# Kernel tuning notes

Measured on AMD Instinct MI355X. Metric: run time of the kernel, lower is better.

Reference implementation:

```python
import jax, jax.numpy as jnp
import numpy as np

A, M, KA, KB = 100000, 200000, 6, 5  # atoms, messages, agraph width, bgraph width
D, DB, H = 256, 256, 256             # atom embed, bond embed, hidden
DEPTH, ATOMS, BONDS = 4, 120, 4


def setup_inputs() -> dict:
    key = jax.random.key(0)
    ks = jax.random.split(key, 14)
    f32 = jnp.float32

    def lin(k, o, i):
        s = 1.0 / np.sqrt(i)
        return jax.random.uniform(k, (o, i), f32, -s, s)

    return dict(
        E_a=jax.random.normal(ks[0], (ATOMS, D), f32) * 0.1,
        E_b=jax.random.normal(ks[1], (BONDS, DB), f32) * 0.1,
        Wz_w=lin(ks[2], H, D + DB + H), Wz_b=jnp.zeros((H,), f32),
        Wr_w=lin(ks[3], H, D + DB),
        Ur_w=lin(ks[4], H, H), Ur_b=jnp.zeros((H,), f32),
        Wh_w=lin(ks[5], H, D + DB + H), Wh_b=jnp.zeros((H,), f32),
        O1_w=lin(ks[6], H, D + H), O1_b=jnp.zeros((H,), f32),
        O2_w=lin(ks[7], H, H), O2_b=jnp.zeros((H,), f32),
        fnode=jax.random.randint(ks[8], (A,), 0, ATOMS),
        fmess_src=jax.random.randint(ks[9], (M,), 0, A),
        fmess_bond=jax.random.randint(ks[10], (M,), 0, BONDS),
        agraph=jax.random.randint(ks[11], (A, KA), 0, M),
        bgraph=jax.random.randint(ks[12], (M, KB), 0, M),
        depth=DEPTH,
    )


def reference(E_a, E_b, Wz_w, Wz_b, Wr_w, Ur_w, Ur_b, Wh_w, Wh_b,
              O1_w, O1_b, O2_w, O2_b,
              fnode, fmess_src, fmess_bond, agraph, bgraph, depth):
    # embed_graph: atom features + message input features
    hnode = E_a[fnode]                                           # [A, D]
    x = jnp.concatenate([hnode[fmess_src], E_b[fmess_bond]], -1)  # [M, D+DB]

    m = x.shape[0]
    h = jnp.zeros((m, Wz_b.shape[0]), x.dtype)                   # [M, H]
    mask = jnp.ones((m, 1), x.dtype).at[0].set(0.0)              # msg 0 = padding
    wr_x = x @ Wr_w.T                                            # loop-invariant

    # GRU message passing (JTNN-style), depthG iterations
    for _ in range(depth):
        h_nei = h[bgraph]                                        # [M, KB, H] gather
        sum_h = h_nei.sum(axis=1)
        z = jax.nn.sigmoid(jnp.concatenate([x, sum_h], -1) @ Wz_w.T + Wz_b)
        r = jax.nn.sigmoid(wr_x[:, None, :] + h_nei @ Ur_w.T + Ur_b)
        sum_gated = (r * h_nei).sum(axis=1)
        pre_h = jnp.tanh(jnp.concatenate([x, sum_gated], -1) @ Wh_w.T + Wh_b)
        h = ((1.0 - z) * sum_h + z * pre_h) * mask

    # mpn tail: gather-sum neighbor messages per atom, concat, outputAtom MLP
    mess_nei = h[agraph].sum(axis=1)                             # [A, H]
    nv = jnp.concatenate([hnode, mess_nei], axis=-1)             # [A, D+H]
    out = jax.nn.relu(nv @ O1_w.T + O1_b) @ O2_w.T + O2_b        # [A, H]
    return out
```

## Files before the change

### kernel.cpp

```cpp
#include <hip/hip_runtime.h>

#define MM 200000
#define AA 100000
#define KA 6
#define KB 5
#define NATOM 120
#define NBOND 4
#define NC (NATOM*NBOND)
#define HH 256
#define HU_B 768

typedef unsigned char  u8;
typedef unsigned short ushort_t;
typedef __attribute__((ext_vector_type(8))) short bf16x8;
typedef __attribute__((ext_vector_type(8))) unsigned short u16x8;
typedef __attribute__((ext_vector_type(4))) float f32x4;
typedef __attribute__((ext_vector_type(2))) float f32x2;
typedef __attribute__((ext_vector_type(4))) unsigned int u32x4;
typedef __attribute__((ext_vector_type(2))) unsigned int u32x2;

#define SBAR() __builtin_amdgcn_sched_barrier(0)

#define OFF_Ea   0
#define OFF_Eb   30720
#define OFF_Wz   31744
#define OFF_Wzb  228352
#define OFF_Wr   228608
#define OFF_Ur   359680
#define OFF_Urb  425216
#define OFF_Wh   425472
#define OFF_Whb  622080
#define OFF_O1   622336
#define OFF_O1b  753408
#define OFF_O2   753664
#define OFF_O2b  819200
#define W_TOTAL  819456

__device__ u8       g_hu0[(size_t)MM*HU_B];
__device__ u8       g_hu1[(size_t)MM*HU_B];
__device__ u8       g_tab[481*HU_B];
__device__ ushort_t g_trb[NC*HH];
__device__ float    g_tz[NC*HH];
__device__ float    g_th[NC*HH];
__device__ float    g_to1[NATOM*HH];
__device__ int      g_cidx[MM];
__device__ ushort_t c_w[W_TOTAL];
__device__ int      g_isf32;

__device__ inline float bf2f(ushort_t u){ return __uint_as_float(((unsigned)u)<<16); }
__device__ inline ushort_t f2bf(float f){
  unsigned u = __float_as_uint(f);
  unsigned r = (u + 0x7FFFu + ((u>>16)&1u)) >> 16;
  return (ushort_t)r;
}
__device__ inline float sigm(float x){
  return __builtin_amdgcn_rcpf(1.0f + __expf(-x));
}
__device__ inline float tanh_f(float x){
  float ax = fabsf(x);
  float e = __expf(-2.0f*ax);
  float t = (1.0f - e) * __builtin_amdgcn_rcpf(1.0f + e);
  return copysignf(t, x);
}
__device__ inline int sidx(int row, int col){ return row*256 + (col ^ ((row&7)<<3)); }

__device__ inline bf16x8 ldsA(const ushort_t* tile, int m0, int lane, int k0){
  int row = m0 + (lane & 15);
  int col = k0 + 8*(lane>>4);
  return *(const bf16x8*)(tile + sidx(row, col));
}
__device__ inline bf16x8 ldgB(const ushort_t* W, int ldw, int koff, int n0, int lane, int k0){
  int n = n0 + (lane & 15);
  int k = koff + k0 + 8*(lane>>4);
  return *(const bf16x8*)(W + n*ldw + k);
}
__device__ inline f32x4 mfma16(bf16x8 a, bf16x8 b, f32x4 c){
  return __builtin_amdgcn_mfma_f32_16x16x32_bf16(a, b, c, 0, 0, 0);
}
__device__ inline void st16(u8* p, const ushort_t* lds_src){
  *(u32x4*)p = *(const u32x4*)lds_src;
}
__device__ inline u32x2 enc_fp8x8(const ushort_t* s){
  u32x2 o;
  int w0 = __builtin_amdgcn_cvt_pk_fp8_f32(bf2f(s[0]), bf2f(s[1]), 0, 0);
  w0     = __builtin_amdgcn_cvt_pk_fp8_f32(bf2f(s[2]), bf2f(s[3]), w0, 1);
  int w1 = __builtin_amdgcn_cvt_pk_fp8_f32(bf2f(s[4]), bf2f(s[5]), 0, 0);
  w1     = __builtin_amdgcn_cvt_pk_fp8_f32(bf2f(s[6]), bf2f(s[7]), w1, 1);
  o.x = (unsigned)w0; o.y = (unsigned)w1;
  return o;
}

__global__ __launch_bounds__(256) void k_detect(const ushort_t* Ea_raw){
  __shared__ int sbad;
  if (threadIdx.x == 0) sbad = 0;
  __syncthreads();
  float v = bf2f(Ea_raw[2*threadIdx.x]);
  float av = fabsf(v);
  int bad = (av > 1e4f) || (av != 0.0f && av < 1e-30f);
  atomicAdd(&sbad, bad);
  __syncthreads();
  if (threadIdx.x == 0) g_isf32 = (sbad > 64) ? 1 : 0;
}

__global__ __launch_bounds__(256) void k_convert(
    const void* Ea, const void* Eb, const void* Wz, const void* Wzb,
    const void* Wr, const void* Ur, const void* Urb, const void* Wh,
    const void* Whb, const void* O1, const void* O1b, const void* O2,
    const void* O2b)
{
  int idx = blockIdx.x*256 + threadIdx.x;
  if (idx >= W_TOTAL) return;
  const void* src; int j;
  if      (idx < OFF_Eb)  { src = Ea;  j = idx - OFF_Ea; }
  else if (idx < OFF_Wz)  { src = Eb;  j = idx - OFF_Eb; }
  else if (idx < OFF_Wzb) { src = Wz;  j = idx - OFF_Wz; }
  else if (idx < OFF_Wr)  { src = Wzb; j = idx - OFF_Wzb; }
  else if (idx < OFF_Ur)  { src = Wr;  j = idx - OFF_Wr; }
  else if (idx < OFF_Urb) { src = Ur;  j = idx - OFF_Ur; }
  else if (idx < OFF_Wh)  { src = Urb; j = idx - OFF_Urb; }
  else if (idx < OFF_Whb) { src = Wh;  j = idx - OFF_Wh; }
  else if (idx < OFF_O1)  { src = Whb; j = idx - OFF_Whb; }
  else if (idx < OFF_O1b) { src = O1;  j = idx - OFF_O1; }
  else if (idx < OFF_O2)  { src = O1b; j = idx - OFF_O1b; }
  else if (idx < OFF_O2b) { src = O2;  j = idx - OFF_O2; }
  else                    { src = O2b; j = idx - OFF_O2b; }
  ushort_t v;
  if (g_isf32) v = f2bf(((const float*)src)[j]);
  else         v = ((const ushort_t*)src)[j];
  c_w[idx] = v;
}

__global__ __launch_bounds__(256) void k_tables()
{
  const ushort_t* Ea  = c_w + OFF_Ea;
  const ushort_t* Eb  = c_w + OFF_Eb;
  int b = blockIdx.x, o = threadIdx.x;
  if (b < 3*NC) {
    int t = b / NC, c = b % NC, a = c >> 2, bd = c & 3;
    const ushort_t* W; const ushort_t* bias; int ldw;
    if (t == 0)      { W = c_w + OFF_Wr; bias = c_w + OFF_Urb; ldw = 512; }
    else if (t == 1) { W = c_w + OFF_Wz; bias = c_w + OFF_Wzb; ldw = 768; }
    else             { W = c_w + OFF_Wh; bias = c_w + OFF_Whb; ldw = 768; }
    float acc = bf2f(bias[o]);
    const ushort_t* wrow = W + o*ldw;
    for (int d = 0; d < 256; d++) acc += bf2f(Ea[a*256+d]) * bf2f(wrow[d]);
    for (int d = 0; d < 256; d++) acc += bf2f(Eb[bd*256+d]) * bf2f(wrow[256+d]);
    if (t == 0)      g_trb[c*256 + o] = f2bf(acc);
    else if (t == 1) g_tz[c*256 + o] = acc;
    else             g_th[c*256 + o] = acc;
  } else {
    int a = b - 3*NC;
    float acc = bf2f(c_w[OFF_O1b + o]);
    const ushort_t* wrow = c_w + OFF_O1 + o*512;
    for (int d = 0; d < 256; d++) acc += bf2f(Ea[a*256+d]) * bf2f(wrow[d]);
    g_to1[a*256 + o] = acc;
  }
}

__global__ __launch_bounds__(256) void k_cidx(const int* fnode, const int* fsrc, const int* fbond){
  int m = blockIdx.x*256 + threadIdx.x;
  if (m >= MM) return;
  g_cidx[m] = fnode[fsrc[m]]*4 + fbond[m];
}

__global__ __launch_bounds__(256) void k_tab0(){
  __shared__ ushort_t sh[256];
  int b = blockIdx.x, o = threadIdx.x;
  u8* row = g_tab + (size_t)b*HU_B;
  if (b == 480){
    ((ushort_t*)row)[o] = 0;
    row[512 + o] = 0;
    return;
  }
  float h = sigm(g_tz[b*256+o]) * tanh_f(g_th[b*256+o]);
  ushort_t hb = f2bf(h);
  ((ushort_t*)row)[o] = hb;
  sh[o] = hb;
  __syncthreads();
  const ushort_t* ur = c_w + OFF_Ur + o*256;
  float acc = 0.f;
  for (int d = 0; d < 256; d++) acc += bf2f(sh[d]) * bf2f(ur[d]);
  int pk = __builtin_amdgcn_cvt_pk_fp8_f32(acc, acc, 0, 0);
  row[512 + o] = (u8)(pk & 0xFF);
}

__global__ __launch_bounds__(256,4) void k_fused(const int* __restrict__ bgraph, int rd, int tbl, int last){
  __shared__ __align__(16) ushort_t sA[32*256];
  __shared__ __align__(16) ushort_t sB[32*256];
  __shared__ int sC[32];
  __shared__ int sJ[32*KB];
  const u8* __restrict__ hup = tbl ? g_tab : (rd ? g_hu1 : g_hu0);
  u8* hun = rd ? g_hu0 : g_hu1;
  const ushort_t* Wz = c_w + OFF_Wz;
  const ushort_t* Wh = c_w + OFF_Wh;
  const ushort_t* Ur = c_w + OFF_Ur;
  int base = blockIdx.x*32, t = threadIdx.x;
  int w = t>>6, lane = t&63;
  int sub = lane & 31, half = lane >> 5;

  if (t < 32)  sC[t] = g_cidx[base + t];
  if (t < 32*KB){
    int j = bgraph[base*KB + t];
    sJ[t] = tbl ? ((j == 0) ? 480 : g_cidx[j]) : j;
  }
  __syncthreads();

  auto issue = [&](int p, bf16x8 (&hv)[KB], u32x2 (&uv)[KB], bf16x8& trv){
    int row = w*8 + 2*p + half;
    trv = *(const bf16x8*)(g_trb + sC[row]*256 + sub*8);
    #pragma unroll
    for (int k = 0; k < KB; k++){
      const u8* rp = hup + (size_t)sJ[row*KB + k]*HU_B;
      hv[k] = *(const bf16x8*)(rp + sub*16);
      uv[k] = *(const u32x2*)(rp + 512 + sub*8);
    }
  };
  auto process = [&](int p, bf16x8 (&hv)[KB], u32x2 (&uv)[KB], bf16x8& trv){
    int row = w*8 + 2*p + half;
    float tre[8];
    #pragma unroll
    for (int e = 0; e < 8; e++) tre[e] = bf2f((ushort_t)trv[e]);
    float sh[8] = {0,0,0,0,0,0,0,0};
    float sg[8] = {0,0,0,0,0,0,0,0};
    #pragma unroll
    for (int k = 0; k < KB; k++){
      f32x2 d0 = __builtin_amdgcn_cvt_pk_f32_fp8(uv[k].x, 0);
      f32x2 d1 = __builtin_amdgcn_cvt_pk_f32_fp8(uv[k].x, 1);
      f32x2 d2 = __builtin_amdgcn_cvt_pk_f32_fp8(uv[k].y, 0);
      f32x2 d3 = __builtin_amdgcn_cvt_pk_f32_fp8(uv[k].y, 1);
      float uvf[8] = {d0.x, d0.y, d1.x, d1.y, d2.x, d2.y, d3.x, d3.y};
      #pragma unroll
      for (int e = 0; e < 8; e++){
        float h = bf2f((ushort_t)hv[k][e]);
        float r = sigm(tre[e] + uvf[e]);
        sh[e] += h;
        sg[e] += r*h;
      }
    }
    u16x8 ph, pg;
    #pragma unroll
    for (int e = 0; e < 8; e++){ ph[e] = f2bf(sh[e]); pg[e] = f2bf(sg[e]); }
    *(u16x8*)(sA + sidx(row, sub*8)) = ph;
    *(u16x8*)(sB + sidx(row, sub*8)) = pg;
  };
  {
    bf16x8 h0[KB], h1[KB];
    u32x2 u0[KB], u1[KB];
    bf16x8 t0v, t1v;
    issue(0, h0, u0, t0v);
    issue(1, h1, u1, t1v);
    SBAR();
    process(0, h0, u0, t0v);
    issue(2, h0, u0, t0v);
    SBAR();
    process(1, h1, u1, t1v);
    issue(3, h1, u1, t1v);
    SBAR();
    process(2, h0, u0, t0v);
    process(3, h1, u1, t1v);
  }
  __syncthreads();

  int n0w = w*64, ln = lane&15, hi = lane>>4;
  f32x4 accz[2][4], acch[2][4];
  #pragma unroll
  for (int i=0;i<2;i++)
    #pragma unroll
    for (int j=0;j<4;j++){ accz[i][j]=(f32x4){0,0,0,0}; acch[i][j]=(f32x4){0,0,0,0}; }
  for (int kt = 0; kt < 8; kt++){
    int k0 = kt*32;
    bf16x8 aF[2], bF[4];
    aF[0] = ldsA(sA, 0, lane, k0);
    aF[1] = ldsA(sA, 16, lane, k0);
    #pragma unroll
    for (int i=0;i<4;i++) bF[i] = ldgB(Wz, 768, 512, n0w + i*16, lane, k0);
    #pragma unroll
    for (int mi=0;mi<2;mi++)
      #pragma unroll
      for (int ni=0;ni<4;ni++) accz[mi][ni] = mfma16(aF[mi], bF[ni], accz[mi][ni]);
  }
  for (int kt = 0; kt < 8; kt++){
    int k0 = kt*32;
    bf16x8 aF[2], bF[4];
    aF[0] = ldsA(sB, 0, lane, k0);
    aF[1] = ldsA(sB, 16, lane, k0);
    #pragma unroll
    for (int i=0;i<4;i++) bF[i] = ldgB(Wh, 768, 512, n0w + i*16, lane, k0);
    #pragma unroll
    for (int mi=0;mi<2;mi++)
      #pragma unroll
      for (int ni=0;ni<4;ni++) acch[mi][ni] = mfma16(aF[mi], bF[ni], acch[mi][ni]);
  }
  __syncthreads();

  #pragma unroll
  for (int mi=0;mi<2;mi++)
    #pragma unroll
    for (int ni=0;ni<4;ni++){
      int col = n0w + ni*16 + ln;
      #pragma unroll
      for (int r=0;r<4;r++){
        int rowl = mi*16 + hi*4 + r;
        int rowg = base + rowl;
        int c = sC[rowl];
        float shv = bf2f(sA[sidx(rowl, col)]);
        float z  = sigm(g_tz[c*256+col] + accz[mi][ni][r]);
        float ph = tanh_f(g_th[c*256+col] + acch[mi][ni][r]);
        float hn = (1.0f - z)*shv + z*ph;
        if (rowg == 0) hn = 0.f;
        sB[sidx(rowl,col)] = f2bf(hn);
      }
    }
  __syncthreads();

  if (!last){
    f32x4 accu[2][4];
    #pragma unroll
    for (int i=0;i<2;i++)
      #pragma unroll
      for (int j=0;j<4;j++) accu[i][j]=(f32x4){0,0,0,0};
    for (int kt = 0; kt < 8; kt++){
      int k0 = kt*32;
      bf16x8 aF[2], bF[4];
      aF[0] = ldsA(sB, 0, lane, k0);
      aF[1] = ldsA(sB, 16, lane, k0);
      #pragma unroll
      for (int i=0;i<4;i++) bF[i] = ldgB(Ur, 256, 0, n0w + i*16, lane, k0);
      #pragma unroll
      for (int mi=0;mi<2;mi++)
        #pragma unroll
        for (int ni=0;ni<4;ni++) accu[mi][ni] = mfma16(aF[mi], bF[ni], accu[mi][ni]);
    }
    #pragma unroll
    for (int mi=0;mi<2;mi++)
      #pragma unroll
      for (int ni=0;ni<4;ni++){
        int col = n0w + ni*16 + ln;
        #pragma unroll
        for (int r=0;r<4;r++){
          int rowl = mi*16 + hi*4 + r;
          sA[sidx(rowl, col)] = f2bf(accu[mi][ni][r]);
        }
      }
    __syncthreads();
  }

  {
    #pragma unroll
    for (int it = 0; it < 4; it++){
      int flat = it*2048 + t*8;
      int row = flat >> 8, col = flat & 255;
      u8* rb = hun + (size_t)(base+row)*HU_B;
      st16(rb + col*2, sB + sidx(row, col));
      if (!last){
        u32x2 enc = enc_fp8x8(sA + sidx(row, col));
        *(u32x2*)(rb + 512 + col) = enc;
      }
    }
  }
}

__global__ __launch_bounds__(256) void k_tail(const int* agraph, const int* fnode,
                                              void* out_v, int rd){
  __shared__ __align__(16) ushort_t sT[64*256];
  const u8* __restrict__ hup = rd ? g_hu1 : g_hu0;
  const ushort_t* O1  = c_w + OFF_O1;
  const ushort_t* O2  = c_w + OFF_O2;
  const ushort_t* O2b = c_w + OFF_O2b;
  int base = blockIdx.x*64, t = threadIdx.x;
  int w = t>>6, lane = t&63;
  int sub = lane & 31, half = lane >> 5;

  auto tissue = [&](int p, bf16x8 (&hv)[KA]){
    int rowl = w*16 + 2*p + half;
    int a = base + rowl;
    int aa = (a < AA) ? a : 0;
    #pragma unroll
    for (int k = 0; k < KA; k++){
      int j = agraph[aa*KA + k];
      hv[k] = *(const bf16x8*)(hup + (size_t)j*HU_B + sub*16);
    }
  };
  auto tproc = [&](int p, bf16x8 (&hv)[KA]){
    int rowl = w*16 + 2*p + half;
    float s[8] = {0,0,0,0,0,0,0,0};
    #pragma unroll
    for (int k = 0; k < KA; k++)
      #pragma unroll
      for (int e = 0; e < 8; e++) s[e] += bf2f((ushort_t)hv[k][e]);
    u16x8 pk;
    #pragma unroll
    for (int e = 0; e < 8; e++) pk[e] = f2bf(s[e]);
    *(u16x8*)(sT + sidx(rowl, sub*8)) = pk;
  };
  {
    bf16x8 b0[KA], b1[KA];
    tissue(0, b0); tissue(1, b1);
    SBAR();
    tproc(0, b0);  tissue(2, b0);
    SBAR();
    tproc(1, b1);  tissue(3, b1);
    SBAR();
    tproc(2, b0);  tissue(4, b0);
    SBAR();
    tproc(3, b1);  tissue(5, b1);
    SBAR();
    tproc(4, b0);  tissue(6, b0);
    SBAR();
    tproc(5, b1);  tissue(7, b1);
    SBAR();
    tproc(6, b0);
    tproc(7, b1);
  }
  __syncthreads();
  int n0w = w*64, ln = lane&15, hi = lane>>4;
  f32x4 acc[4][4];
  #pragma unroll
  for (int i=0;i<4;i++)
    #pragma unroll
    for (int j=0;j<4;j++) acc[i][j]=(f32x4){0,0,0,0};
  for (int kt = 0; kt < 8; kt++){
    int k0 = kt*32;
    bf16x8 aF[4], bF[4];
    #pragma unroll
    for (int i=0;i<4;i++) aF[i] = ldsA(sT, i*16, lane, k0);
    #pragma unroll
    for (int i=0;i<4;i++) bF[i] = ldgB(O1, 512, 256, n0w + i*16, lane, k0);
    #pragma unroll
    for (int mi=0;mi<4;mi++)
      #pragma unroll
      for (int ni=0;ni<4;ni++) acc[mi][ni] = mfma16(aF[mi], bF[ni], acc[mi][ni]);
  }
  __syncthreads();
  #pragma unroll
  for (int mi=0;mi<4;mi++)
    #pragma unroll
    for (int ni=0;ni<4;ni++){
      int col = n0w + ni*16 + ln;
      #pragma unroll
      for (int r=0;r<4;r++){
        int rowl = mi*16 + hi*4 + r;
        int a = base + rowl;
        int tt = (a < AA) ? fnode[a] : 0;
        float pre = g_to1[tt*256+col] + acc[mi][ni][r];
        sT[sidx(rowl,col)] = f2bf(fmaxf(pre, 0.f));
      }
    }
  __syncthreads();
  f32x4 acco[4][4];
  #pragma unroll
  for (int i=0;i<4;i++)
    #pragma unroll
    for (int j=0;j<4;j++) acco[i][j]=(f32x4){0,0,0,0};
  for (int kt = 0; kt < 8; kt++){
    int k0 = kt*32;
    bf16x8 aF[4], bF[4];
    #pragma unroll
    for (int i=0;i<4;i++) aF[i] = ldsA(sT, i*16, lane, k0);
    #pragma unroll
    for (int i=0;i<4;i++) bF[i] = ldgB(O2, 256, 0, n0w + i*16, lane, k0);
    #pragma unroll
    for (int mi=0;mi<4;mi++)
      #pragma unroll
      for (int ni=0;ni<4;ni++) acco[mi][ni] = mfma16(aF[mi], bF[ni], acco[mi][ni]);
  }
  int isf32 = g_isf32;
  #pragma unroll
  for (int mi=0;mi<4;mi++)
    #pragma unroll
    for (int ni=0;ni<4;ni++){
      int col = n0w + ni*16 + ln;
      float bias = bf2f(O2b[col]);
      #pragma unroll
      for (int r=0;r<4;r++){
        int rowg = base + mi*16 + hi*4 + r;
        if (rowg < AA){
          float v = acco[mi][ni][r] + bias;
          if (isf32) ((float*)out_v)[(size_t)rowg*256 + col] = v;
          else       ((ushort_t*)out_v)[(size_t)rowg*256 + col] = f2bf(v);
        }
      }
    }
}

extern "C" void kernel_launch(void* const* d_in, const int* in_sizes, int n_in,
                              void* d_out, int out_size, void* d_ws, size_t ws_size,
                              hipStream_t stream) {
  const int* fnode = (const int*)d_in[13];
  const int* fsrc  = (const int*)d_in[14];
  const int* fbond = (const int*)d_in[15];
  const int* agraph = (const int*)d_in[16];
  const int* bgraph = (const int*)d_in[17];

  k_detect<<<1, 256, 0, stream>>>((const ushort_t*)d_in[0]);
  k_convert<<<(W_TOTAL + 255)/256, 256, 0, stream>>>(
      d_in[0], d_in[1], d_in[2], d_in[3], d_in[4], d_in[5], d_in[6],
      d_in[7], d_in[8], d_in[9], d_in[10], d_in[11], d_in[12]);
  k_tables<<<3*NC + NATOM, 256, 0, stream>>>();
  k_cidx<<<(MM + 255)/256, 256, 0, stream>>>(fnode, fsrc, fbond);
  k_tab0<<<481, 256, 0, stream>>>();
  k_fused<<<MM/32, 256, 0, stream>>>(bgraph, 1, 1, 0);
  k_fused<<<MM/32, 256, 0, stream>>>(bgraph, 0, 0, 0);
  k_fused<<<MM/32, 256, 0, stream>>>(bgraph, 1, 0, 1);
  k_tail<<<(AA + 63)/64, 256, 0, stream>>>(agraph, fnode, (void*)d_out, 0);
}
```

Baseline: 1.368 ms.

## Replace pull-gather of neighbor messages with push-scatter into per-slot expanded buffers

Builds a reverse CSR (count, scan, fill) of the bgraph and agraph neighbor slots. Each fused GRU step now writes its new message rows directly into every consumer slot of an expanded buffer, so the next step and the tail read contiguous rows instead of doing random gathers. This trades scattered reads for scattered writes: total bytes written grow by roughly KB times, the intermediate buffers become very large, and four extra preprocessing kernels with atomics are added. The per-warp write loop over a variable-degree list may also be imbalanced.

```diff
diff --git a/kernel.cpp b/kernel.cpp
--- a/kernel.cpp
+++ b/kernel.cpp
@@ -9,6 +9,8 @@
 #define NC (NATOM*NBOND)
 #define HH 256
 #define HU_B 768
+#define NS_B (MM*KB)
+#define NS_A (AA*KA)
 
 typedef unsigned char  u8;
 typedef unsigned short ushort_t;
@@ -36,8 +38,9 @@
 #define OFF_O2b  819200
 #define W_TOTAL  819456
 
-__device__ u8       g_hu0[(size_t)MM*HU_B];
-__device__ u8       g_hu1[(size_t)MM*HU_B];
+__device__ u8       g_exp0[(size_t)NS_B*HU_B];
+__device__ u8       g_exp1[(size_t)NS_B*HU_B];
+__device__ u8       g_texp[(size_t)NS_A*512];
 __device__ u8       g_tab[481*HU_B];
 __device__ ushort_t g_trb[NC*HH];
 __device__ float    g_tz[NC*HH];
@@ -46,6 +49,9 @@
 __device__ int      g_cidx[MM];
 __device__ ushort_t c_w[W_TOTAL];
 __device__ int      g_isf32;
+__device__ int      g_boff[MM], g_bcnt[MM], g_bsl[NS_B];
+__device__ int      g_aoff[MM], g_acnt[MM], g_asl[NS_A];
+__device__ int      g_cur[2];
 
 __device__ inline float bf2f(ushort_t u){ return __uint_as_float(((unsigned)u)<<16); }
 __device__ inline ushort_t f2bf(float f){
@@ -76,18 +82,6 @@
 }
 __device__ inline f32x4 mfma16(bf16x8 a, bf16x8 b, f32x4 c){
   return __builtin_amdgcn_mfma_f32_16x16x32_bf16(a, b, c, 0, 0, 0);
-}
-__device__ inline void st16(u8* p, const ushort_t* lds_src){
-  *(u32x4*)p = *(const u32x4*)lds_src;
-}
-__device__ inline u32x2 enc_fp8x8(const ushort_t* s){
-  u32x2 o;
-  int w0 = __builtin_amdgcn_cvt_pk_fp8_f32(bf2f(s[0]), bf2f(s[1]), 0, 0);
-  w0     = __builtin_amdgcn_cvt_pk_fp8_f32(bf2f(s[2]), bf2f(s[3]), w0, 1);
-  int w1 = __builtin_amdgcn_cvt_pk_fp8_f32(bf2f(s[4]), bf2f(s[5]), 0, 0);
-  w1     = __builtin_amdgcn_cvt_pk_fp8_f32(bf2f(s[6]), bf2f(s[7]), w1, 1);
-  o.x = (unsigned)w0; o.y = (unsigned)w1;
-  return o;
 }
 
 __global__ __launch_bounds__(256) void k_detect(const ushort_t* Ea_raw){
@@ -163,6 +157,62 @@
   g_cidx[m] = fnode[fsrc[m]]*4 + fbond[m];
 }
 
+__global__ __launch_bounds__(256) void k_zero(){
+  int m = blockIdx.x*256 + threadIdx.x;
+  if (m < MM){ g_bcnt[m] = 0; g_acnt[m] = 0; }
+  if (m == 0){ g_cur[0] = 0; g_cur[1] = 0; }
+}
+__global__ __launch_bounds__(256) void k_count(const int* bgraph, const int* agraph){
+  int s = blockIdx.x*256 + threadIdx.x;
+  if (s < NS_B) atomicAdd(&g_bcnt[bgraph[s]], 1);
+  else if (s < NS_B + NS_A) atomicAdd(&g_acnt[agraph[s - NS_B]], 1);
+}
+__global__ __launch_bounds__(256) void k_alloc(){
+  int j = blockIdx.x*256 + threadIdx.x;
+  int lane = threadIdx.x & 63;
+  {
+    int c = (j < MM) ? g_bcnt[j] : 0;
+    int incl = c;
+    #pragma unroll
+    for (int d = 1; d < 64; d <<= 1){
+      int n = __shfl_up(incl, d);
+      if (lane >= d) incl += n;
+    }
+    int wtot = __shfl(incl, 63);
+    int wbase = 0;
+    if (lane == 63) wbase = atomicAdd(&g_cur[0], wtot);
+    wbase = __shfl(wbase, 63);
+    if (j < MM){ g_boff[j] = wbase + incl - c; g_bcnt[j] = 0; }
+  }
+  {
+    int c = (j < MM) ? g_acnt[j] : 0;
+    int incl = c;
+    #pragma unroll
+    for (int d = 1; d < 64; d <<= 1){
+      int n = __shfl_up(incl, d);
+      if (lane >= d) incl += n;
+    }
+    int wtot = __shfl(incl, 63);
+    int wbase = 0;
+    if (lane == 63) wbase = atomicAdd(&g_cur[1], wtot);
+    wbase = __shfl(wbase, 63);
+    if (j < MM){ g_aoff[j] = wbase + incl - c; g_acnt[j] = 0; }
+  }
+}
+__global__ __launch_bounds__(256) void k_fill(const int* bgraph, const int* agraph){
+  int s = blockIdx.x*256 + threadIdx.x;
+  if (s < NS_B){
+    int j = bgraph[s];
+    int p = atomicAdd(&g_bcnt[j], 1);
+    g_bsl[g_boff[j] + p] = s;
+  } else if (s < NS_B + NS_A){
+    int s2 = s - NS_B;
+    int j = agraph[s2];
+    int p = atomicAdd(&g_acnt[j], 1);
+    g_asl[g_aoff[j] + p] = s2;
+  }
+}
+
 __global__ __launch_bounds__(256) void k_tab0(){
   __shared__ ushort_t sh[256];
   int b = blockIdx.x, o = threadIdx.x;
@@ -189,8 +239,8 @@
   __shared__ __align__(16) ushort_t sB[32*256];
   __shared__ int sC[32];
   __shared__ int sJ[32*KB];
-  const u8* __restrict__ hup = tbl ? g_tab : (rd ? g_hu1 : g_hu0);
-  u8* hun = rd ? g_hu0 : g_hu1;
+  const u8* __restrict__ src = rd ? g_exp1 : g_exp0;
+  u8* dst = rd ? g_exp0 : g_exp1;
   const ushort_t* Wz = c_w + OFF_Wz;
   const ushort_t* Wh = c_w + OFF_Wh;
   const ushort_t* Ur = c_w + OFF_Ur;
@@ -199,20 +249,29 @@
   int sub = lane & 31, half = lane >> 5;
 
   if (t < 32)  sC[t] = g_cidx[base + t];
-  if (t < 32*KB){
+  if (tbl && t < 32*KB){
     int j = bgraph[base*KB + t];
-    sJ[t] = tbl ? ((j == 0) ? 480 : g_cidx[j]) : j;
+    sJ[t] = (j == 0) ? 480 : g_cidx[j];
   }
   __syncthreads();
 
   auto issue = [&](int p, bf16x8 (&hv)[KB], u32x2 (&uv)[KB], bf16x8& trv){
     int row = w*8 + 2*p + half;
     trv = *(const bf16x8*)(g_trb + sC[row]*256 + sub*8);
-    #pragma unroll
-    for (int k = 0; k < KB; k++){
-      const u8* rp = hup + (size_t)sJ[row*KB + k]*HU_B;
-      hv[k] = *(const bf16x8*)(rp + sub*16);
-      uv[k] = *(const u32x2*)(rp + 512 + sub*8);
+    if (tbl){
+      #pragma unroll
+      for (int k = 0; k < KB; k++){
+        const u8* rp = g_tab + (size_t)sJ[row*KB + k]*HU_B;
+        hv[k] = *(const bf16x8*)(rp + sub*16);
+        uv[k] = *(const u32x2*)(rp + 512 + sub*8);
+      }
+    } else {
+      const u8* rp0 = src + ((size_t)(base+row)*KB)*HU_B;
+      #pragma unroll
+      for (int k = 0; k < KB; k++){
+        hv[k] = *(const bf16x8*)(rp0 + (size_t)k*HU_B + sub*16);
+        uv[k] = *(const u32x2*)(rp0 + (size_t)k*HU_B + 512 + sub*8);
+      }
     }
   };
   auto process = [&](int p, bf16x8 (&hv)[KB], u32x2 (&uv)[KB], bf16x8& trv){
@@ -313,6 +372,8 @@
     }
   __syncthreads();
 
+  u8* sUb = (u8*)sA;
+
   if (!last){
     f32x4 accu[2][4];
     #pragma unroll
@@ -339,31 +400,42 @@
         #pragma unroll
         for (int r=0;r<4;r++){
           int rowl = mi*16 + hi*4 + r;
-          sA[sidx(rowl, col)] = f2bf(accu[mi][ni][r]);
+          float v = accu[mi][ni][r];
+          int pk = __builtin_amdgcn_cvt_pk_fp8_f32(v, v, 0, 0);
+          sUb[rowl*256 + col] = (u8)(pk & 0xFF);
         }
       }
     __syncthreads();
-  }
-
-  {
-    #pragma unroll
-    for (int it = 0; it < 4; it++){
-      int flat = it*2048 + t*8;
-      int row = flat >> 8, col = flat & 255;
-      u8* rb = hun + (size_t)(base+row)*HU_B;
-      st16(rb + col*2, sB + sidx(row, col));
-      if (!last){
-        u32x2 enc = enc_fp8x8(sA + sidx(row, col));
-        *(u32x2*)(rb + 512 + col) = enc;
-      }
-    }
-  }
-}
-
-__global__ __launch_bounds__(256) void k_tail(const int* agraph, const int* fnode,
-                                              void* out_v, int rd){
+
+    for (int i = 0; i < 8; i++){
+      int rowl = w*8 + i;
+      int j = base + rowl;
+      int off = g_boff[j], deg = g_bcnt[j];
+      for (int d = 0; d < deg; d++){
+        size_t slot = (size_t)g_bsl[off + d];
+        u8* dp = dst + slot*HU_B;
+        if (lane < 32)
+          *(u32x4*)(dp + (size_t)lane*16) = *(const u32x4*)(sB + sidx(rowl, lane*8));
+        else if (lane < 48)
+          *(u32x4*)(dp + 512 + (size_t)(lane-32)*16) = *(const u32x4*)(sUb + rowl*256 + (lane-32)*16);
+      }
+    }
+  } else {
+    for (int i = 0; i < 8; i++){
+      int rowl = w*8 + i;
+      int j = base + rowl;
+      int off = g_aoff[j], deg = g_acnt[j];
+      for (int d = 0; d < deg; d++){
+        size_t slot = (size_t)g_asl[off + d];
+        if (lane < 32)
+          *(u32x4*)(g_texp + slot*512 + (size_t)lane*16) = *(const u32x4*)(sB + sidx(rowl, lane*8));
+      }
+    }
+  }
+}
+
+__global__ __launch_bounds__(256) void k_tail(const int* fnode, void* out_v){
   __shared__ __align__(16) ushort_t sT[64*256];
-  const u8* __restrict__ hup = rd ? g_hu1 : g_hu0;
   const ushort_t* O1  = c_w + OFF_O1;
   const ushort_t* O2  = c_w + OFF_O2;
   const ushort_t* O2b = c_w + OFF_O2b;
@@ -375,11 +447,10 @@
     int rowl = w*16 + 2*p + half;
     int a = base + rowl;
     int aa = (a < AA) ? a : 0;
-    #pragma unroll
-    for (int k = 0; k < KA; k++){
-      int j = agraph[aa*KA + k];
-      hv[k] = *(const bf16x8*)(hup + (size_t)j*HU_B + sub*16);
-    }
+    const u8* rp0 = g_texp + (size_t)aa*KA*512;
+    #pragma unroll
+    for (int k = 0; k < KA; k++)
+      hv[k] = *(const bf16x8*)(rp0 + (size_t)k*512 + sub*16);
   };
   auto tproc = [&](int p, bf16x8 (&hv)[KA]){
     int rowl = w*16 + 2*p + half;
@@ -498,9 +569,13 @@
       d_in[7], d_in[8], d_in[9], d_in[10], d_in[11], d_in[12]);
   k_tables<<<3*NC + NATOM, 256, 0, stream>>>();
   k_cidx<<<(MM + 255)/256, 256, 0, stream>>>(fnode, fsrc, fbond);
+  k_zero<<<(MM + 255)/256, 256, 0, stream>>>();
+  k_count<<<(NS_B + NS_A + 255)/256, 256, 0, stream>>>(bgraph, agraph);
+  k_alloc<<<(MM + 255)/256, 256, 0, stream>>>();
+  k_fill<<<(NS_B + NS_A + 255)/256, 256, 0, stream>>>(bgraph, agraph);
   k_tab0<<<481, 256, 0, stream>>>();
   k_fused<<<MM/32, 256, 0, stream>>>(bgraph, 1, 1, 0);
   k_fused<<<MM/32, 256, 0, stream>>>(bgraph, 0, 0, 0);
   k_fused<<<MM/32, 256, 0, stream>>>(bgraph, 1, 0, 1);
-  k_tail<<<(AA + 63)/64, 256, 0, stream>>>(agraph, fnode, (void*)d_out, 0);
-}
+  k_tail<<<(AA + 63)/64, 256, 0, stream>>>(fnode, (void*)d_out);
+}
```

Measured after the change: 2.121 ms. 1.55x slower.
